# Performance work log

Measured on AMD Instinct MI355X. Metric: run time of the kernel, lower is better.

The kernel has to match this reference:

```python
import jax, jax.numpy as jnp
import numpy as np

EMB = 1024      # EMBEDDING_DIM == INPUT_SIZE
HID = 1024      # HIDDEN_SIZE
TEXT_V = 50257
EMOJI_V = 64
SEQ = 2048
NEMO = 16
LABELS = 7


def setup_inputs() -> dict:
    key = jax.random.key(0)
    ks = jax.random.split(key, 10)
    s = lambda k, shape: (jax.random.normal(k, shape, dtype=jnp.float32) * 0.02)
    return dict(
        sentence_ids=jax.random.randint(ks[0], (SEQ,), 0, TEXT_V),
        emoji_ids=jax.random.randint(ks[1], (NEMO,), 0, EMOJI_V),
        word_emb=s(ks[2], (TEXT_V, EMB)),
        emoji_emb=s(ks[3], (EMOJI_V, EMB)),
        attn_W=s(ks[4], (1, HID + EMB)),
        attn_b=jnp.zeros((1,), jnp.float32),
        comb_W=s(ks[5], (EMB, 2 * EMB)),
        comb_b=jnp.zeros((EMB,), jnp.float32),
        W_ih=s(ks[6], (4 * HID, EMB)),
        W_hh=s(ks[7], (4 * HID, HID)),
        b_ih=jnp.zeros((4 * HID,), jnp.float32),
        b_hh=jnp.zeros((4 * HID,), jnp.float32),
        out_W=s(ks[8], (LABELS, HID)),
        out_b=jnp.zeros((LABELS,), jnp.float32),
    )


def reference(sentence_ids, emoji_ids, word_emb, emoji_emb, attn_W, attn_b,
              comb_W, comb_b, W_ih, W_hh, b_ih, b_hh, out_W, out_b):
    # emoji context vector: mean of emoji embeddings over the emoji axis -> [EMB]
    emoji_ave = jnp.mean(emoji_emb[emoji_ids], axis=0)
    sent = word_emb[sentence_ids]  # [SEQ, EMB], batch dim of 1 is implicit

    def step(carry, x):
        h, c = carry  # [HID], [HID]
        # Bahdanau-style attention: softmax over a single logit == 1.0 (faithful)
        logit = attn_W @ jnp.concatenate([x, h]) + attn_b            # [1]
        w = jax.nn.softmax(logit)                                     # [1]
        attn_applied = w[0] * emoji_ave                               # [EMB]
        combined = jax.nn.relu(
            comb_W @ jnp.concatenate([x, attn_applied]) + comb_b)    # [EMB]
        # single-step LSTM cell, PyTorch gate order (i, f, g, o)
        gates = W_ih @ combined + b_ih + W_hh @ h + b_hh              # [4*HID]
        i, f, g, o = jnp.split(gates, 4)
        c_new = jax.nn.sigmoid(f) * c + jax.nn.sigmoid(i) * jnp.tanh(g)
        h_new = jax.nn.sigmoid(o) * jnp.tanh(c_new)
        return (h_new, c_new), None

    h0 = jnp.zeros((HID,), sent.dtype)
    (h, c), _ = jax.lax.scan(step, (h0, h0), sent)
    out = out_W @ h + out_b  # hidden2label on last lstm_out
    return out[None, :]      # [1, LABEL_SIZE]
```

## Files before the change

kernel.cpp:

```cpp
#include <hip/hip_runtime.h>
#include <hip/hip_bf16.h>
#include <stdint.h>
#include <math.h>

#define SEQ    2048
#define EMB    1024
#define HID    1024
#define G4     4096
#define NEMO   16
#define NLAB   7

#define NB 128

__device__ __forceinline__ float sigf(float x) { return 1.0f / (1.0f + expf(-x)); }

__global__ void k_init(const int* __restrict__ emoji_ids,
                       const float* __restrict__ emoji_emb,
                       float* __restrict__ eave,
                       unsigned long long* __restrict__ htag)
{
    int t = threadIdx.x;
    int ids[NEMO];
#pragma unroll
    for (int n = 0; n < NEMO; ++n) ids[n] = emoji_ids[n];
    for (int e = t; e < EMB; e += 256) {
        float s = 0.f;
#pragma unroll
        for (int n = 0; n < NEMO; ++n) s += emoji_emb[(size_t)ids[n] * EMB + e];
        eave[e] = s * (1.0f / 16.0f);
    }
    for (int i = t; i < 2 * HID; i += 256) htag[i] = 0ull;
}

__global__ void k_cvec(const float* __restrict__ combW,
                       const float* __restrict__ combB,
                       const float* __restrict__ eave,
                       float* __restrict__ cvec)
{
    int gw   = (blockIdx.x * 256 + threadIdx.x) >> 6;
    int lane = threadIdx.x & 63;
#pragma unroll
    for (int rr = 0; rr < 4; ++rr) {
        int r = gw * 4 + rr;
        const float* wrow = combW + (size_t)r * 2048 + 1024;
        float s = 0.f;
        for (int k = lane; k < EMB; k += 64) s = fmaf(wrow[k], eave[k], s);
#pragma unroll
        for (int off = 1; off < 64; off <<= 1) s += __shfl_xor(s, off);
        if (lane == 0) cvec[r] = s + combB[r];
    }
}

__global__ __launch_bounds__(256) void k_gemm(
    const float* __restrict__ Asrc,
    const int*   __restrict__ ids,
    const float* __restrict__ emb,
    const float* __restrict__ B, int bstride,
    const float* __restrict__ bias1,
    const float* __restrict__ bias2,
    float* __restrict__ O, int N, int relu)
{
    __shared__ float As[16][128];
    __shared__ float Bs[16][128];
    const int tid  = threadIdx.x;
    const int row0 = blockIdx.y * 128;
    const int col0 = blockIdx.x * 128;
    const int lr = tid >> 2;
    const int kq = tid & 3;
    const float *ar0, *ar1;
    if (ids) {
        ar0 = emb + (size_t)ids[row0 + lr]      * 1024;
        ar1 = emb + (size_t)ids[row0 + lr + 64] * 1024;
    } else {
        ar0 = Asrc + (size_t)(row0 + lr)      * 1024;
        ar1 = Asrc + (size_t)(row0 + lr + 64) * 1024;
    }
    const float* br0 = B + (size_t)(col0 + lr)      * bstride;
    const float* br1 = B + (size_t)(col0 + lr + 64) * bstride;
    const int tx = tid & 15, ty = tid >> 4;

    float acc[8][8];
#pragma unroll
    for (int i = 0; i < 8; ++i)
#pragma unroll
        for (int j = 0; j < 8; ++j) acc[i][j] = 0.f;

    for (int k0 = 0; k0 < 1024; k0 += 16) {
        float4 a0 = *(const float4*)(ar0 + k0 + kq * 4);
        float4 a1 = *(const float4*)(ar1 + k0 + kq * 4);
        float4 b0 = *(const float4*)(br0 + k0 + kq * 4);
        float4 b1 = *(const float4*)(br1 + k0 + kq * 4);
        __syncthreads();
        {
            const float* pa0 = &a0.x; const float* pa1 = &a1.x;
            const float* pb0 = &b0.x; const float* pb1 = &b1.x;
#pragma unroll
            for (int e = 0; e < 4; ++e) {
                As[kq * 4 + e][lr]      = pa0[e];
                As[kq * 4 + e][lr + 64] = pa1[e];
                Bs[kq * 4 + e][lr]      = pb0[e];
                Bs[kq * 4 + e][lr + 64] = pb1[e];
            }
        }
        __syncthreads();
#pragma unroll
        for (int kk = 0; kk < 16; ++kk) {
            float af[8], bf[8];
            *(float4*)(af)     = *(const float4*)&As[kk][ty * 8];
            *(float4*)(af + 4) = *(const float4*)&As[kk][ty * 8 + 4];
            *(float4*)(bf)     = *(const float4*)&Bs[kk][tx * 8];
            *(float4*)(bf + 4) = *(const float4*)&Bs[kk][tx * 8 + 4];
#pragma unroll
            for (int i = 0; i < 8; ++i)
#pragma unroll
                for (int j = 0; j < 8; ++j)
                    acc[i][j] = fmaf(af[i], bf[j], acc[i][j]);
        }
    }
    float bv[8];
    *(float4*)(bv)     = *(const float4*)&bias1[col0 + tx * 8];
    *(float4*)(bv + 4) = *(const float4*)&bias1[col0 + tx * 8 + 4];
    if (bias2) {
        float b2[8];
        *(float4*)(b2)     = *(const float4*)&bias2[col0 + tx * 8];
        *(float4*)(b2 + 4) = *(const float4*)&bias2[col0 + tx * 8 + 4];
#pragma unroll
        for (int j = 0; j < 8; ++j) bv[j] += b2[j];
    }
#pragma unroll
    for (int i = 0; i < 8; ++i) {
        int m = row0 + ty * 8 + i;
        float o[8];
#pragma unroll
        for (int j = 0; j < 8; ++j) {
            float v = acc[i][j] + bv[j];
            o[j] = relu ? fmaxf(v, 0.f) : v;
        }
        *(float4*)&O[(size_t)m * N + col0 + tx * 8]     = *(float4*)(o);
        *(float4*)&O[(size_t)m * N + col0 + tx * 8 + 4] = *(float4*)(o + 4);
    }
}

__global__ __launch_bounds__(256, 1) void k_lstm(
    const float* __restrict__ Whh,
    const float* __restrict__ Gin,
    unsigned long long* __restrict__ htag)
{
    const int b    = blockIdx.x;
    const int t    = threadIdx.x;
    const int lane = t & 63;
    const int wv   = t >> 6;

    float w[8][16];
#pragma unroll
    for (int i = 0; i < 8; ++i) {
        int r = wv + 4 * i;
        int grow = ((r >> 3) << 10) + (b << 3) + (r & 7);
        const float4* p = (const float4*)(Whh + (size_t)grow * HID + lane * 16);
#pragma unroll
        for (int q = 0; q < 4; ++q) {
            float4 a = p[q];
            w[i][4 * q + 0] = a.x; w[i][4 * q + 1] = a.y;
            w[i][4 * q + 2] = a.z; w[i][4 * q + 3] = a.w;
        }
    }

    __shared__ float4 hl4[256];
    __shared__ float  red[32 * 72];
    __shared__ float  gat[32];
    __shared__ float  cst[8];
    if (t < 8) cst[t] = 0.f;

    const int s_j4 = t & 3, s_col = t >> 2;
    const int rr = t >> 3, kk = t & 7;
    const int growR = ((rr >> 3) << 10) + (b << 3) + (rr & 7);
    unsigned long long* myslots0 = htag + 4 * t;

    for (int s = 0; s < SEQ; ++s) {
        float gval = 0.f;
        if (kk == 0) gval = Gin[(size_t)s * G4 + growR];

        unsigned long long* src = myslots0 + (size_t)(((unsigned)(s + 1)) & 1u) * HID;
        const unsigned expw = (unsigned)s;
        unsigned long long v0, v1, v2, v3;
        for (;;) {
            v0 = __hip_atomic_load(src + 0, __ATOMIC_RELAXED, __HIP_MEMORY_SCOPE_AGENT);
            v1 = __hip_atomic_load(src + 1, __ATOMIC_RELAXED, __HIP_MEMORY_SCOPE_AGENT);
            v2 = __hip_atomic_load(src + 2, __ATOMIC_RELAXED, __HIP_MEMORY_SCOPE_AGENT);
            v3 = __hip_atomic_load(src + 3, __ATOMIC_RELAXED, __HIP_MEMORY_SCOPE_AGENT);
            int ok = ((unsigned)(v0 >> 32) == expw) & ((unsigned)(v1 >> 32) == expw) &
                     ((unsigned)(v2 >> 32) == expw) & ((unsigned)(v3 >> 32) == expw);
            if (__all(ok)) break;
        }
        hl4[s_j4 * 64 + s_col] = make_float4(
            __uint_as_float((unsigned)v0), __uint_as_float((unsigned)v1),
            __uint_as_float((unsigned)v2), __uint_as_float((unsigned)v3));
        __syncthreads();

        float hf[16];
#pragma unroll
        for (int q = 0; q < 4; ++q) {
            float4 hv = hl4[q * 64 + lane];
            hf[4 * q + 0] = hv.x; hf[4 * q + 1] = hv.y;
            hf[4 * q + 2] = hv.z; hf[4 * q + 3] = hv.w;
        }
        float p[8];
#pragma unroll
        for (int i = 0; i < 8; ++i) p[i] = 0.f;
#pragma unroll
        for (int j = 0; j < 16; ++j)
#pragma unroll
            for (int i = 0; i < 8; ++i)
                p[i] = fmaf(w[i][j], hf[j], p[i]);
#pragma unroll
        for (int i = 0; i < 8; ++i) red[(wv + 4 * i) * 72 + lane] = p[i];
        __syncthreads();

        float rs = 0.f;
#pragma unroll
        for (int j = 0; j < 8; ++j) rs += red[rr * 72 + j * 8 + kk];
        rs += __shfl_xor(rs, 1);
        rs += __shfl_xor(rs, 2);
        rs += __shfl_xor(rs, 4);
        if (kk == 0) gat[rr] = rs + gval;
        __syncthreads();

        if (t < 8) {
            float gi = gat[t], gf = gat[8 + t], gg = gat[16 + t], go = gat[24 + t];
            float c = sigf(gf) * cst[t] + sigf(gi) * tanhf(gg);
            cst[t] = c;
            float h = sigf(go) * tanhf(c);
            unsigned long long pk =
                ((unsigned long long)(unsigned)(s + 1) << 32) |
                (unsigned long long)__float_as_uint(h);
            __hip_atomic_store(htag + (size_t)(((unsigned)s) & 1u) * HID + b * 8 + t,
                               pk, __ATOMIC_RELAXED, __HIP_MEMORY_SCOPE_AGENT);
        }
    }
}

__global__ void k_out(const float* __restrict__ outW,
                      const float* __restrict__ outb,
                      const unsigned long long* __restrict__ htag,
                      float* __restrict__ out)
{
    int wv = threadIdx.x >> 6, lane = threadIdx.x & 63;
    if (wv < NLAB) {
        float s = 0.f;
        for (int k = lane; k < HID; k += 64) {
            float h = __uint_as_float((unsigned)(htag[HID + k] & 0xffffffffULL));
            s = fmaf(outW[wv * HID + k], h, s);
        }
#pragma unroll
        for (int off = 1; off < 64; off <<= 1) s += __shfl_xor(s, off);
        if (lane == 0) out[wv] = s + outb[wv];
    }
}

extern "C" void kernel_launch(void* const* d_in, const int* in_sizes, int n_in,
                              void* d_out, int out_size, void* d_ws, size_t ws_size,
                              hipStream_t stream)
{
    const int*   sent_ids = (const int*)  d_in[0];
    const int*   emo_ids  = (const int*)  d_in[1];
    const float* word_emb = (const float*)d_in[2];
    const float* emo_emb  = (const float*)d_in[3];
    const float* comb_W   = (const float*)d_in[6];
    const float* comb_b   = (const float*)d_in[7];
    const float* W_ih     = (const float*)d_in[8];
    const float* W_hh     = (const float*)d_in[9];
    const float* b_ih     = (const float*)d_in[10];
    const float* b_hh     = (const float*)d_in[11];
    const float* out_W    = (const float*)d_in[12];
    const float* out_b    = (const float*)d_in[13];
    float* out = (float*)d_out;

    float* ws   = (float*)d_ws;
    float* eave = ws;
    float* cvec = ws + 1024;
    float* C    = ws + 4096;
    float* G    = ws + 4096 + (size_t)SEQ * EMB;
    unsigned long long* htag =
        (unsigned long long*)(ws + 4096 + (size_t)SEQ * EMB + (size_t)SEQ * G4);

    k_init<<<1, 256, 0, stream>>>(emo_ids, emo_emb, eave, htag);
    k_cvec<<<64, 256, 0, stream>>>(comb_W, comb_b, eave, cvec);
    dim3 g1(EMB / 128, SEQ / 128);
    k_gemm<<<g1, 256, 0, stream>>>(nullptr, sent_ids, word_emb,
                                   comb_W, 2048, cvec, nullptr, C, EMB, 1);
    dim3 g2(G4 / 128, SEQ / 128);
    k_gemm<<<g2, 256, 0, stream>>>(C, nullptr, nullptr,
                                   W_ih, 1024, b_ih, b_hh, G, G4, 0);
    k_lstm<<<NB, 256, 0, stream>>>(W_hh, G, htag);
    k_out<<<1, 448, 0, stream>>>(out_W, out_b, htag, out);
}
```

Measured before the change: 4.983 ms.

## Fuse projection GEMMs and LSTM recurrence into one persistent kernel with progress flags

Merges the two input-projection GEMMs and the LSTM recurrence into a single launch. Block ranges are assigned to the comb GEMM, the W_ih GEMM and the LSTM. Per-row-block progress counters let the second GEMM start on rows of C as soon as they are done, and let the LSTM consume G one 128-step chunk at a time. The aim is to remove kernel launch gaps and to overlap the tail of the GEMM work with the start of the sequential recurrence. In exchange it adds spin-waits, atomic (coherent) loads on the A operand and on G, and depends on in-order block dispatch to avoid stalls.

```diff
diff --git a/kernel.cpp b/kernel.cpp
--- a/kernel.cpp
+++ b/kernel.cpp
@@ -10,14 +10,31 @@
 #define NEMO   16
 #define NLAB   7
 
-#define NB 128
+#define NB_C    128
+#define NB_G    512
+#define NB_LSTM 128
+#define CBLK_PER_ROW 8u
+#define GBLK_PER_ROW 32u
 
 __device__ __forceinline__ float sigf(float x) { return 1.0f / (1.0f + expf(-x)); }
+
+__device__ __forceinline__ float4 aload16(const float* p)
+{
+    unsigned long long u0 = __hip_atomic_load((const unsigned long long*)p,
+                                              __ATOMIC_RELAXED, __HIP_MEMORY_SCOPE_AGENT);
+    unsigned long long u1 = __hip_atomic_load((const unsigned long long*)(p + 2),
+                                              __ATOMIC_RELAXED, __HIP_MEMORY_SCOPE_AGENT);
+    return make_float4(__uint_as_float((unsigned)u0),
+                       __uint_as_float((unsigned)(u0 >> 32)),
+                       __uint_as_float((unsigned)u1),
+                       __uint_as_float((unsigned)(u1 >> 32)));
+}
 
 __global__ void k_init(const int* __restrict__ emoji_ids,
                        const float* __restrict__ emoji_emb,
                        float* __restrict__ eave,
-                       unsigned long long* __restrict__ htag)
+                       unsigned long long* __restrict__ htag,
+                       unsigned* __restrict__ prog)
 {
     int t = threadIdx.x;
     int ids[NEMO];
@@ -30,6 +47,7 @@
         eave[e] = s * (1.0f / 16.0f);
     }
     for (int i = t; i < 2 * HID; i += 256) htag[i] = 0ull;
+    if (t < 32) prog[t] = 0u;
 }
 
 __global__ void k_cvec(const float* __restrict__ combW,
@@ -51,103 +69,143 @@
     }
 }
 
-__global__ __launch_bounds__(256) void k_gemm(
-    const float* __restrict__ Asrc,
-    const int*   __restrict__ ids,
-    const float* __restrict__ emb,
-    const float* __restrict__ B, int bstride,
-    const float* __restrict__ bias1,
-    const float* __restrict__ bias2,
-    float* __restrict__ O, int N, int relu)
-{
-    __shared__ float As[16][128];
-    __shared__ float Bs[16][128];
-    const int tid  = threadIdx.x;
-    const int row0 = blockIdx.y * 128;
-    const int col0 = blockIdx.x * 128;
-    const int lr = tid >> 2;
-    const int kq = tid & 3;
-    const float *ar0, *ar1;
-    if (ids) {
-        ar0 = emb + (size_t)ids[row0 + lr]      * 1024;
-        ar1 = emb + (size_t)ids[row0 + lr + 64] * 1024;
-    } else {
-        ar0 = Asrc + (size_t)(row0 + lr)      * 1024;
-        ar1 = Asrc + (size_t)(row0 + lr + 64) * 1024;
-    }
-    const float* br0 = B + (size_t)(col0 + lr)      * bstride;
-    const float* br1 = B + (size_t)(col0 + lr + 64) * bstride;
-    const int tx = tid & 15, ty = tid >> 4;
-
-    float acc[8][8];
-#pragma unroll
-    for (int i = 0; i < 8; ++i)
-#pragma unroll
-        for (int j = 0; j < 8; ++j) acc[i][j] = 0.f;
-
-    for (int k0 = 0; k0 < 1024; k0 += 16) {
-        float4 a0 = *(const float4*)(ar0 + k0 + kq * 4);
-        float4 a1 = *(const float4*)(ar1 + k0 + kq * 4);
-        float4 b0 = *(const float4*)(br0 + k0 + kq * 4);
-        float4 b1 = *(const float4*)(br1 + k0 + kq * 4);
+__global__ __launch_bounds__(256, 1) void k_fused(
+    const int*   sent_ids,
+    const float* word_emb,
+    const float* comb_W,
+    const float* cvec,
+    float*       C,
+    const float* W_ih,
+    const float* b_ih,
+    const float* b_hh,
+    float*       G,
+    const float* Whh,
+    unsigned long long* htag,
+    unsigned*    progC,
+    unsigned*    progG)
+{
+    __shared__ float smem[4096];
+    const int bid = blockIdx.x;
+    const int t   = threadIdx.x;
+
+    if (bid < NB_C + NB_G) {
+        const float* Asrc; const int* ids;
+        const float* Bm; int bstride;
+        const float* bias1; const float* bias2;
+        float* O; int N; int relu; int bx, by;
+        if (bid < NB_C) {
+            by = bid >> 3; bx = bid & 7;
+            Asrc = nullptr; ids = sent_ids;
+            Bm = comb_W; bstride = 2048;
+            bias1 = cvec; bias2 = nullptr;
+            O = C; N = EMB; relu = 1;
+        } else {
+            const int idx = bid - NB_C;
+            by = idx >> 5; bx = idx & 31;
+            if (t == 0) {
+                while (__hip_atomic_load(progC + by, __ATOMIC_ACQUIRE,
+                                         __HIP_MEMORY_SCOPE_AGENT) != CBLK_PER_ROW) {}
+            }
+            __syncthreads();
+            Asrc = C; ids = nullptr;
+            Bm = W_ih; bstride = 1024;
+            bias1 = b_ih; bias2 = b_hh;
+            O = G; N = G4; relu = 0;
+        }
+
+        float* As_ = smem;
+        float* Bs_ = smem + 2048;
+        const int row0 = by * 128;
+        const int col0 = bx * 128;
+        const int lr = t >> 2;
+        const int kq = t & 3;
+        const float *ar0, *ar1;
+        if (ids) {
+            ar0 = word_emb + (size_t)ids[row0 + lr]      * 1024;
+            ar1 = word_emb + (size_t)ids[row0 + lr + 64] * 1024;
+        } else {
+            ar0 = Asrc + (size_t)(row0 + lr)      * 1024;
+            ar1 = Asrc + (size_t)(row0 + lr + 64) * 1024;
+        }
+        const float* br0 = Bm + (size_t)(col0 + lr)      * bstride;
+        const float* br1 = Bm + (size_t)(col0 + lr + 64) * bstride;
+        const int tx = t & 15, ty = t >> 4;
+
+        float acc[8][8];
+#pragma unroll
+        for (int i = 0; i < 8; ++i)
+#pragma unroll
+            for (int j = 0; j < 8; ++j) acc[i][j] = 0.f;
+
+        for (int k0 = 0; k0 < 1024; k0 += 16) {
+            float4 a0 = aload16(ar0 + k0 + kq * 4);
+            float4 a1 = aload16(ar1 + k0 + kq * 4);
+            float4 b0 = *(const float4*)(br0 + k0 + kq * 4);
+            float4 b1 = *(const float4*)(br1 + k0 + kq * 4);
+            __syncthreads();
+            {
+                const float* pa0 = &a0.x; const float* pa1 = &a1.x;
+                const float* pb0 = &b0.x; const float* pb1 = &b1.x;
+#pragma unroll
+                for (int e = 0; e < 4; ++e) {
+                    As_[(kq * 4 + e) * 128 + lr]      = pa0[e];
+                    As_[(kq * 4 + e) * 128 + lr + 64] = pa1[e];
+                    Bs_[(kq * 4 + e) * 128 + lr]      = pb0[e];
+                    Bs_[(kq * 4 + e) * 128 + lr + 64] = pb1[e];
+                }
+            }
+            __syncthreads();
+#pragma unroll
+            for (int kk = 0; kk < 16; ++kk) {
+                float af[8], bf[8];
+                *(float4*)(af)     = *(const float4*)&As_[kk * 128 + ty * 8];
+                *(float4*)(af + 4) = *(const float4*)&As_[kk * 128 + ty * 8 + 4];
+                *(float4*)(bf)     = *(const float4*)&Bs_[kk * 128 + tx * 8];
+                *(float4*)(bf + 4) = *(const float4*)&Bs_[kk * 128 + tx * 8 + 4];
+#pragma unroll
+                for (int i = 0; i < 8; ++i)
+#pragma unroll
+                    for (int j = 0; j < 8; ++j)
+                        acc[i][j] = fmaf(af[i], bf[j], acc[i][j]);
+            }
+        }
+        float bv[8];
+        *(float4*)(bv)     = *(const float4*)&bias1[col0 + tx * 8];
+        *(float4*)(bv + 4) = *(const float4*)&bias1[col0 + tx * 8 + 4];
+        if (bias2) {
+            float b2[8];
+            *(float4*)(b2)     = *(const float4*)&bias2[col0 + tx * 8];
+            *(float4*)(b2 + 4) = *(const float4*)&bias2[col0 + tx * 8 + 4];
+#pragma unroll
+            for (int j = 0; j < 8; ++j) bv[j] += b2[j];
+        }
+#pragma unroll
+        for (int i = 0; i < 8; ++i) {
+            int m = row0 + ty * 8 + i;
+            float o[8];
+#pragma unroll
+            for (int j = 0; j < 8; ++j) {
+                float v = acc[i][j] + bv[j];
+                o[j] = relu ? fmaxf(v, 0.f) : v;
+            }
+            *(float4*)&O[(size_t)m * N + col0 + tx * 8]     = *(float4*)(o);
+            *(float4*)&O[(size_t)m * N + col0 + tx * 8 + 4] = *(float4*)(o + 4);
+        }
+
         __syncthreads();
-        {
-            const float* pa0 = &a0.x; const float* pa1 = &a1.x;
-            const float* pb0 = &b0.x; const float* pb1 = &b1.x;
-#pragma unroll
-            for (int e = 0; e < 4; ++e) {
-                As[kq * 4 + e][lr]      = pa0[e];
-                As[kq * 4 + e][lr + 64] = pa1[e];
-                Bs[kq * 4 + e][lr]      = pb0[e];
-                Bs[kq * 4 + e][lr + 64] = pb1[e];
-            }
-        }
-        __syncthreads();
-#pragma unroll
-        for (int kk = 0; kk < 16; ++kk) {
-            float af[8], bf[8];
-            *(float4*)(af)     = *(const float4*)&As[kk][ty * 8];
-            *(float4*)(af + 4) = *(const float4*)&As[kk][ty * 8 + 4];
-            *(float4*)(bf)     = *(const float4*)&Bs[kk][tx * 8];
-            *(float4*)(bf + 4) = *(const float4*)&Bs[kk][tx * 8 + 4];
-#pragma unroll
-            for (int i = 0; i < 8; ++i)
-#pragma unroll
-                for (int j = 0; j < 8; ++j)
-                    acc[i][j] = fmaf(af[i], bf[j], acc[i][j]);
-        }
-    }
-    float bv[8];
-    *(float4*)(bv)     = *(const float4*)&bias1[col0 + tx * 8];
-    *(float4*)(bv + 4) = *(const float4*)&bias1[col0 + tx * 8 + 4];
-    if (bias2) {
-        float b2[8];
-        *(float4*)(b2)     = *(const float4*)&bias2[col0 + tx * 8];
-        *(float4*)(b2 + 4) = *(const float4*)&bias2[col0 + tx * 8 + 4];
-#pragma unroll
-        for (int j = 0; j < 8; ++j) bv[j] += b2[j];
-    }
-#pragma unroll
-    for (int i = 0; i < 8; ++i) {
-        int m = row0 + ty * 8 + i;
-        float o[8];
-#pragma unroll
-        for (int j = 0; j < 8; ++j) {
-            float v = acc[i][j] + bv[j];
-            o[j] = relu ? fmaxf(v, 0.f) : v;
-        }
-        *(float4*)&O[(size_t)m * N + col0 + tx * 8]     = *(float4*)(o);
-        *(float4*)&O[(size_t)m * N + col0 + tx * 8 + 4] = *(float4*)(o + 4);
-    }
-}
-
-__global__ __launch_bounds__(256, 1) void k_lstm(
-    const float* __restrict__ Whh,
-    const float* __restrict__ Gin,
-    unsigned long long* __restrict__ htag)
-{
-    const int b    = blockIdx.x;
-    const int t    = threadIdx.x;
+        if (t == 0) {
+            __threadfence();
+            if (bid < NB_C)
+                __hip_atomic_fetch_add(progC + by, 1u, __ATOMIC_RELEASE,
+                                       __HIP_MEMORY_SCOPE_AGENT);
+            else
+                __hip_atomic_fetch_add(progG + by, 1u, __ATOMIC_RELEASE,
+                                       __HIP_MEMORY_SCOPE_AGENT);
+        }
+        return;
+    }
+
+    const int b    = bid - (NB_C + NB_G);
     const int lane = t & 63;
     const int wv   = t >> 6;
 
@@ -165,10 +223,10 @@
         }
     }
 
-    __shared__ float4 hl4[256];
-    __shared__ float  red[32 * 72];
-    __shared__ float  gat[32];
-    __shared__ float  cst[8];
+    float4* hl4 = (float4*)smem;
+    float*  red = smem + 1024;
+    float*  gat = smem + 1024 + 2304;
+    float*  cst = smem + 1024 + 2304 + 32;
     if (t < 8) cst[t] = 0.f;
 
     const int s_j4 = t & 3, s_col = t >> 2;
@@ -176,9 +234,26 @@
     const int growR = ((rr >> 3) << 10) + (b << 3) + (rr & 7);
     unsigned long long* myslots0 = htag + 4 * t;
 
+    int rb_ready = 0;
+
     for (int s = 0; s < SEQ; ++s) {
+        const int rb = s >> 7;
+        if (rb >= rb_ready) {
+            if (t == 0) {
+                while (__hip_atomic_load(progG + rb, __ATOMIC_ACQUIRE,
+                                         __HIP_MEMORY_SCOPE_AGENT) != GBLK_PER_ROW) {}
+            }
+            __syncthreads();
+            rb_ready = rb + 1;
+        }
+
         float gval = 0.f;
-        if (kk == 0) gval = Gin[(size_t)s * G4 + growR];
+        if (kk == 0) {
+            unsigned gu = __hip_atomic_load(
+                (const unsigned*)(G + (size_t)s * G4 + growR),
+                __ATOMIC_RELAXED, __HIP_MEMORY_SCOPE_AGENT);
+            gval = __uint_as_float(gu);
+        }
 
         unsigned long long* src = myslots0 + (size_t)(((unsigned)(s + 1)) & 1u) * HID;
         const unsigned expw = (unsigned)s;
@@ -282,15 +357,14 @@
     float* G    = ws + 4096 + (size_t)SEQ * EMB;
     unsigned long long* htag =
         (unsigned long long*)(ws + 4096 + (size_t)SEQ * EMB + (size_t)SEQ * G4);
-
-    k_init<<<1, 256, 0, stream>>>(emo_ids, emo_emb, eave, htag);
+    unsigned* prog  = (unsigned*)(htag + 2 * HID);
+    unsigned* progC = prog;
+    unsigned* progG = prog + 16;
+
+    k_init<<<1, 256, 0, stream>>>(emo_ids, emo_emb, eave, htag, prog);
     k_cvec<<<64, 256, 0, stream>>>(comb_W, comb_b, eave, cvec);
-    dim3 g1(EMB / 128, SEQ / 128);
-    k_gemm<<<g1, 256, 0, stream>>>(nullptr, sent_ids, word_emb,
-                                   comb_W, 2048, cvec, nullptr, C, EMB, 1);
-    dim3 g2(G4 / 128, SEQ / 128);
-    k_gemm<<<g2, 256, 0, stream>>>(C, nullptr, nullptr,
-                                   W_ih, 1024, b_ih, b_hh, G, G4, 0);
-    k_lstm<<<NB, 256, 0, stream>>>(W_hh, G, htag);
+    k_fused<<<NB_C + NB_G + NB_LSTM, 256, 0, stream>>>(
+        sent_ids, word_emb, comb_W, cvec, C, W_ih, b_ih, b_hh, G, W_hh,
+        htag, progC, progG);
     k_out<<<1, 448, 0, stream>>>(out_W, out_b, htag, out);
 }
```

New measurement: 5.343 ms. 7.2% more time.
